# Kernel optimization log

Hardware: AMD Instinct MI355X
Metric: run time of the kernel (lower is better)

Reference implementation:

```python
import jax, jax.numpy as jnp
import numpy as np

BASE_RES = 16
SCENE_MIN = np.array([-1.0, -1.0, -1.0], dtype=np.float32)
SCENE_MAX = np.array([1.0, 1.0, 1.0], dtype=np.float32)
MAX_HITS = 100  # width of intersection_indices, per CPU fallback
EPS = 1e-8


def setup_inputs() -> dict:
    key = jax.random.key(0)
    k1, k2, k3, k4 = jax.random.split(key, 4)
    R = 4096
    scene_min = jnp.asarray(SCENE_MIN)
    scene_max = jnp.asarray(SCENE_MAX)
    scene_size = scene_max - scene_min

    # --- voxel grid, as in _initialize_base_voxels ---
    lin = (jnp.arange(BASE_RES, dtype=jnp.float32) + 0.5) / BASE_RES
    xx, yy, zz = jnp.meshgrid(lin, lin, lin, indexing='ij')
    positions = jnp.stack([xx, yy, zz], axis=-1).reshape(-1, 3)  # [V,3] in [0,1]
    positions = positions * scene_size + scene_min
    V = positions.shape[0]
    voxel_size = scene_size.max() / BASE_RES
    voxel_sizes = jnp.full((V,), voxel_size, dtype=jnp.float32)
    voxel_densities = jax.random.normal(k1, (V,), dtype=jnp.float32) * 0.1
    voxel_colors = jax.random.uniform(k2, (V, 3), dtype=jnp.float32) * 0.5 + 0.25

    # --- rays: origins near a camera point outside the scene, normalized directions ---
    ray_origins = jax.random.uniform(k3, (R, 3), dtype=jnp.float32) * 0.2 + jnp.array([0.0, 0.0, -2.5])
    dirs = jax.random.normal(k4, (R, 3), dtype=jnp.float32) * 0.3 + jnp.array([0.0, 0.0, 1.0])
    ray_directions = dirs / jnp.linalg.norm(dirs, axis=-1, keepdims=True)

    return {
        'ray_origins': ray_origins,
        'ray_directions': ray_directions,
        'voxel_positions': positions,
        'voxel_sizes': voxel_sizes,
        'voxel_densities': voxel_densities,
        'voxel_colors': voxel_colors,
    }


def _composite(ray_origins, ray_directions, voxel_positions, voxel_sizes,
               voxel_densities, voxel_colors):
    # ray-AABB slab test against every voxel cube
    o = ray_origins[:, None, :]                       # [R,1,3]
    d = ray_directions[:, None, :]                    # [R,1,3]
    safe_d = jnp.where(jnp.abs(d) < EPS, jnp.where(d >= 0, EPS, -EPS), d)
    inv_d = 1.0 / safe_d
    half = (voxel_sizes * 0.5)[None, :, None]         # [1,V,1]
    ctr = voxel_positions[None, :, :]                 # [1,V,3]
    t0 = (ctr - half - o) * inv_d                     # [R,V,3]
    t1 = (ctr + half - o) * inv_d
    t_near = jnp.max(jnp.minimum(t0, t1), axis=-1)    # [R,V]
    t_far = jnp.min(jnp.maximum(t0, t1), axis=-1)
    t_near = jnp.maximum(t_near, 0.0)
    hit = t_far > t_near                              # [R,V] bool

    # sort intersections along each ray by entry distance; misses to the back
    sort_key = jnp.where(hit, t_near, jnp.inf)
    order = jnp.argsort(sort_key, axis=1)             # [R,V] int
    tn_s = jnp.take_along_axis(t_near, order, axis=1)
    tf_s = jnp.take_along_axis(t_far, order, axis=1)
    hit_s = jnp.take_along_axis(hit, order, axis=1)

    sigma = jnp.exp(voxel_densities)                  # raw density -> sigma (as in pruning)
    sigma_s = jnp.take_along_axis(jnp.broadcast_to(sigma[None, :], hit.shape), order, axis=1)
    colors_s = jnp.take_along_axis(
        jnp.broadcast_to(voxel_colors[None, :, :], hit.shape + (3,)),
        order[:, :, None], axis=1)                    # [R,V,3]

    dt = jnp.where(hit_s, tf_s - tn_s, 0.0)
    alpha = jnp.where(hit_s, 1.0 - jnp.exp(-sigma_s * dt), 0.0)  # [R,V]
    # exclusive cumulative transmittance
    trans = jnp.cumprod(1.0 - alpha + 1e-10, axis=1)
    trans = jnp.concatenate([jnp.ones_like(trans[:, :1]), trans[:, :-1]], axis=1)
    w = trans * alpha                                 # [R,V]

    rgb = jnp.einsum('rv,rvc->rc', w, colors_s)       # [R,3]
    t_mid = 0.5 * (tn_s + tf_s)
    depth = jnp.sum(w * jnp.where(hit_s, t_mid, 0.0), axis=1)  # [R]

    counts = jnp.sum(hit, axis=1).astype(jnp.int32)   # [R]
    idx100 = jnp.where(hit_s[:, :MAX_HITS], order[:, :MAX_HITS], 0).astype(jnp.int32)
    return rgb, depth, counts, idx100


def reference(ray_origins, ray_directions, voxel_positions, voxel_sizes,
              voxel_densities, voxel_colors):
    rgb, depth, counts, idx = _composite(
        ray_origins, ray_directions, voxel_positions, voxel_sizes,
        voxel_densities, voxel_colors)
    return rgb, depth, counts, idx
```

## Files before the change

### kernel.cpp

```cpp
#include <hip/hip_runtime.h>
#include <math.h>


#define MAXH 100

__global__ __launch_bounds__(256)
void svr_pack(const float* __restrict__ vdens,
              const float* __restrict__ vcol,
              float4* __restrict__ vox,
              float4* __restrict__ idx_region)
{
    int t = blockIdx.x * blockDim.x + threadIdx.x;
    if (t < 4096) {
        float4 p;
        p.x = vcol[t * 3 + 0];
        p.y = vcol[t * 3 + 1];
        p.z = vcol[t * 3 + 2];
        p.w = expf(vdens[t]);
        vox[t] = p;
    }
    idx_region[t] = make_float4(0.f, 0.f, 0.f, 0.f);
}

__global__ __launch_bounds__(64)
void svraster_dda(const float* __restrict__ ro,
                  const float* __restrict__ rd,
                  const float4* __restrict__ vox,
                  float* __restrict__ out, int R)
{
    const int r = blockIdx.x * 64 + threadIdx.x;
    if (r >= R) return;

    float o0 = ro[r*3+0], o1 = ro[r*3+1], o2 = ro[r*3+2];
    float d0 = rd[r*3+0], d1 = rd[r*3+1], d2 = rd[r*3+2];
    d0 = (fabsf(d0) < 1e-8f) ? ((d0 >= 0.f) ? 1e-8f : -1e-8f) : d0;
    d1 = (fabsf(d1) < 1e-8f) ? ((d1 >= 0.f) ? 1e-8f : -1e-8f) : d1;
    d2 = (fabsf(d2) < 1e-8f) ? ((d2 >= 0.f) ? 1e-8f : -1e-8f) : d2;
    const float i0 = 1.0f / d0, i1 = 1.0f / d1, i2 = 1.0f / d2;

    float a0 = (-1.f - o0) * i0, b0 = (1.f - o0) * i0;
    float a1 = (-1.f - o1) * i1, b1 = (1.f - o1) * i1;
    float a2 = (-1.f - o2) * i2, b2 = (1.f - o2) * i2;
    float tlo = fmaxf(fmaxf(fminf(a0,b0), fminf(a1,b1)), fminf(a2,b2));
    tlo = fmaxf(tlo, 0.f);
    float thi = fminf(fminf(fmaxf(a0,b0), fmaxf(a1,b1)), fmaxf(a2,b2));

    float Tr = 1.f, cr = 0.f, cg = 0.f, cb = 0.f, depth = 0.f;
    int count = 0;
    float* oidx = out + (size_t)5 * R + (size_t)r * MAXH;

    if (thi > tlo) {
        float px = o0 + tlo * d0, py = o1 + tlo * d1, pz = o2 + tlo * d2;
        int c0 = (int)floorf((px + 1.f) * 8.f); c0 = c0 < 0 ? 0 : (c0 > 15 ? 15 : c0);
        int c1 = (int)floorf((py + 1.f) * 8.f); c1 = c1 < 0 ? 0 : (c1 > 15 ? 15 : c1);
        int c2c = (int)floorf((pz + 1.f) * 8.f); c2c = c2c < 0 ? 0 : (c2c > 15 ? 15 : c2c);

        const int s0 = (i0 > 0.f) ? 1 : -1;
        const int s1 = (i1 > 0.f) ? 1 : -1;
        const int s2 = (i2 > 0.f) ? 1 : -1;
        const float db0 = 0.125f * (float)s0;
        const float db1 = 0.125f * (float)s1;
        const float db2 = 0.125f * (float)s2;

        float bx0 = -1.f + 0.125f * (float)(c0  + (s0 > 0 ? 1 : 0));
        float bx1 = -1.f + 0.125f * (float)(c1  + (s1 > 0 ? 1 : 0));
        float bx2 = -1.f + 0.125f * (float)(c2c + (s2 > 0 ? 1 : 0));
        float tn0 = ((bx0 - db0) - o0) * i0;
        float tn1 = ((bx1 - db1) - o1) * i1;
        float tn2 = ((bx2 - db2) - o2) * i2;
        float tf0 = (bx0 - o0) * i0;
        float tf1 = (bx1 - o1) * i1;
        float tf2 = (bx2 - o2) * i2;

        for (int it = 0; it < 64; ++it) {
            float tn = fmaxf(fmaxf(fmaxf(tn0, tn1), tn2), 0.f);
            float tf = fminf(fminf(tf0, tf1), tf2);
            if (tf > tn) {
                int vid = (c0 << 8) | (c1 << 4) | c2c;
                float4 vx = vox[vid];
                float dt = tf - tn;
                float alpha = 1.0f - expf(-vx.w * dt);
                float w = Tr * alpha;
                cr += w * vx.x;
                cg += w * vx.y;
                cb += w * vx.z;
                depth += w * 0.5f * (tn + tf);
                Tr *= (1.0f - alpha + 1e-10f);
                oidx[count] = (float)vid;
                ++count;
            }
            bool ax = (tf0 <= tf1) & (tf0 <= tf2);
            bool ay = (!ax) & (tf1 <= tf2);
            bool az = !(ax | ay);
            int n0 = c0  + (ax ? s0 : 0);
            int n1 = c1  + (ay ? s1 : 0);
            int n2 = c2c + (az ? s2 : 0);
            if (((n0 | n1 | n2) & ~15) != 0) break;
            c0 = n0; c1 = n1; c2c = n2;
            tn0 = ax ? tf0 : tn0;
            tn1 = ay ? tf1 : tn1;
            tn2 = az ? tf2 : tn2;
            bx0 = ax ? (bx0 + db0) : bx0;
            bx1 = ay ? (bx1 + db1) : bx1;
            bx2 = az ? (bx2 + db2) : bx2;
            tf0 = ax ? ((bx0 - o0) * i0) : tf0;
            tf1 = ay ? ((bx1 - o1) * i1) : tf1;
            tf2 = az ? ((bx2 - o2) * i2) : tf2;
        }
    }

    out[r * 3 + 0] = cr;
    out[r * 3 + 1] = cg;
    out[r * 3 + 2] = cb;
    out[(size_t)3 * R + r] = depth;
    out[(size_t)4 * R + r] = (float)count;
}

extern "C" void kernel_launch(void* const* d_in, const int* in_sizes, int n_in,
                              void* d_out, int out_size, void* d_ws, size_t ws_size,
                              hipStream_t stream) {
    const float* ro    = (const float*)d_in[0];
    const float* rd    = (const float*)d_in[1];
    const float* vdens = (const float*)d_in[4];
    const float* vcol  = (const float*)d_in[5];
    float* out = (float*)d_out;
    float4* vox = (float4*)d_ws;

    const int R = in_sizes[0] / 3;
    float4* idx_region = (float4*)(out + (size_t)5 * R);

    hipLaunchKernelGGL(svr_pack, dim3(400), dim3(256), 0, stream,
                       vdens, vcol, vox, idx_region);
    hipLaunchKernelGGL(svraster_dda, dim3(R / 64), dim3(64), 0, stream,
                       ro, rd, vox, out, R);
}
```

Measured before the change: 75.56 us.

## Fuse voxel packing and DDA into one kernel with LDS voxel table and prefetch

Merges the pack kernel and the ray-marching kernel into a single launch. Each 256-thread block recomputes the 4096-entry voxel table (color plus exp(density)) into 64 KB of shared memory and zeroes its own rays' index rows. The DDA loop now loads the next voxel before compositing the current one, hiding LDS latency. This removes a launch and the workspace round trip, but every block redoes the 4096 exps. With only 16 blocks for 4096 rays, each block's 64 KB of LDS and the fewer, larger blocks could leave most CUs idle.

```diff
diff --git a/kernel.cpp b/kernel.cpp
--- a/kernel.cpp
+++ b/kernel.cpp
@@ -5,30 +5,35 @@
 #define MAXH 100
 
 __global__ __launch_bounds__(256)
-void svr_pack(const float* __restrict__ vdens,
-              const float* __restrict__ vcol,
-              float4* __restrict__ vox,
-              float4* __restrict__ idx_region)
+void svr_fused(const float* __restrict__ ro,
+               const float* __restrict__ rd,
+               const float* __restrict__ vdens,
+               const float* __restrict__ vcol,
+               float* __restrict__ out, int R)
 {
-    int t = blockIdx.x * blockDim.x + threadIdx.x;
-    if (t < 4096) {
+    __shared__ float4 vox[4096];
+    const int tid = threadIdx.x;
+    const int r = blockIdx.x * 256 + tid;
+
+#pragma unroll
+    for (int i = 0; i < 16; ++i) {
+        int v = i * 256 + tid;
         float4 p;
-        p.x = vcol[t * 3 + 0];
-        p.y = vcol[t * 3 + 1];
-        p.z = vcol[t * 3 + 2];
-        p.w = expf(vdens[t]);
-        vox[t] = p;
+        p.x = vcol[v * 3 + 0];
+        p.y = vcol[v * 3 + 1];
+        p.z = vcol[v * 3 + 2];
+        p.w = expf(vdens[v]);
+        vox[v] = p;
     }
-    idx_region[t] = make_float4(0.f, 0.f, 0.f, 0.f);
-}
 
-__global__ __launch_bounds__(64)
-void svraster_dda(const float* __restrict__ ro,
-                  const float* __restrict__ rd,
-                  const float4* __restrict__ vox,
-                  float* __restrict__ out, int R)
-{
-    const int r = blockIdx.x * 64 + threadIdx.x;
+    float* oidx = out + (size_t)5 * R + (size_t)r * MAXH;
+    if (r < R) {
+        float4* oidx4 = (float4*)oidx;
+#pragma unroll
+        for (int i = 0; i < 25; ++i) oidx4[i] = make_float4(0.f, 0.f, 0.f, 0.f);
+    }
+
+    __syncthreads();
     if (r >= R) return;
 
     float o0 = ro[r*3+0], o1 = ro[r*3+1], o2 = ro[r*3+2];
@@ -47,7 +52,6 @@
 
     float Tr = 1.f, cr = 0.f, cg = 0.f, cb = 0.f, depth = 0.f;
     int count = 0;
-    float* oidx = out + (size_t)5 * R + (size_t)r * MAXH;
 
     if (thi > tlo) {
         float px = o0 + tlo * d0, py = o1 + tlo * d1, pz = o2 + tlo * d2;
@@ -72,14 +76,26 @@
         float tf1 = (bx1 - o1) * i1;
         float tf2 = (bx2 - o2) * i2;
 
+        int vid = (c0 << 8) | (c1 << 4) | c2c;
+        float4 vx = vox[vid];
+
         for (int it = 0; it < 64; ++it) {
             float tn = fmaxf(fmaxf(fmaxf(tn0, tn1), tn2), 0.f);
             float tf = fminf(fminf(tf0, tf1), tf2);
+
+            bool ax = (tf0 <= tf1) & (tf0 <= tf2);
+            bool ay = (!ax) & (tf1 <= tf2);
+            bool az = !(ax | ay);
+            int n0 = c0  + (ax ? s0 : 0);
+            int n1 = c1  + (ay ? s1 : 0);
+            int n2 = c2c + (az ? s2 : 0);
+            bool inside = (((n0 | n1 | n2) & ~15) == 0);
+            int nvid = (n0 << 8) | (n1 << 4) | n2;
+            float4 nvx;
+            if (inside) nvx = vox[nvid];
+
             if (tf > tn) {
-                int vid = (c0 << 8) | (c1 << 4) | c2c;
-                float4 vx = vox[vid];
-                float dt = tf - tn;
-                float alpha = 1.0f - expf(-vx.w * dt);
+                float alpha = 1.0f - expf(-vx.w * (tf - tn));
                 float w = Tr * alpha;
                 cr += w * vx.x;
                 cg += w * vx.y;
@@ -89,14 +105,9 @@
                 oidx[count] = (float)vid;
                 ++count;
             }
-            bool ax = (tf0 <= tf1) & (tf0 <= tf2);
-            bool ay = (!ax) & (tf1 <= tf2);
-            bool az = !(ax | ay);
-            int n0 = c0  + (ax ? s0 : 0);
-            int n1 = c1  + (ay ? s1 : 0);
-            int n2 = c2c + (az ? s2 : 0);
-            if (((n0 | n1 | n2) & ~15) != 0) break;
-            c0 = n0; c1 = n1; c2c = n2;
+            if (!inside) break;
+
+            c0 = n0; c1 = n1; c2c = n2; vid = nvid; vx = nvx;
             tn0 = ax ? tf0 : tn0;
             tn1 = ay ? tf1 : tn1;
             tn2 = az ? tf2 : tn2;
@@ -124,13 +135,8 @@
     const float* vdens = (const float*)d_in[4];
     const float* vcol  = (const float*)d_in[5];
     float* out = (float*)d_out;
-    float4* vox = (float4*)d_ws;
 
     const int R = in_sizes[0] / 3;
-    float4* idx_region = (float4*)(out + (size_t)5 * R);
-
-    hipLaunchKernelGGL(svr_pack, dim3(400), dim3(256), 0, stream,
-                       vdens, vcol, vox, idx_region);
-    hipLaunchKernelGGL(svraster_dda, dim3(R / 64), dim3(64), 0, stream,
-                       ro, rd, vox, out, R);
+    hipLaunchKernelGGL(svr_fused, dim3((R + 255) / 256), dim3(256), 0, stream,
+                       ro, rd, vdens, vcol, out, R);
 }
```

Result: faster. 73.16 us (-3.2%).
